# Optimization experiments

Measured on AMD Instinct MI355X. Metric: run time of the kernel, lower is better.

## Reference

```python
import jax, jax.numpy as jnp
import numpy as np

B, S, D = 2, 2048, 2048
H, HD = 16, 128
P = 2048  # past (cached) kv length


def setup_inputs() -> dict:
    key = jax.random.key(0)
    ks = jax.random.split(key, 12)
    sw = 1.0 / np.sqrt(D)
    inp = {
        "x": jax.random.normal(ks[0], (B, S, D), jnp.float32),
        "past_k": jax.random.normal(ks[1], (B, H, P, HD), jnp.float32),
        "past_v": jax.random.normal(ks[2], (B, H, P, HD), jnp.float32),
        "Wq": jax.random.normal(ks[3], (D, D), jnp.float32) * sw,
        "bq": jax.random.normal(ks[4], (D,), jnp.float32) * 0.01,
        "Wk": jax.random.normal(ks[5], (D, D), jnp.float32) * sw,
        "bk": jax.random.normal(ks[6], (D,), jnp.float32) * 0.01,
        "Wv": jax.random.normal(ks[7], (D, D), jnp.float32) * sw,
        "bv": jax.random.normal(ks[8], (D,), jnp.float32) * 0.01,
        "Wo": jax.random.normal(ks[9], (D, D), jnp.float32) * sw,
        "bo": jax.random.normal(ks[10], (D,), jnp.float32) * 0.01,
    }
    return inp


def _heads(t):
    # [B, S, D] -> [B, H, S, HD]
    return t.reshape(B, -1, H, HD).transpose(0, 2, 1, 3)


def reference(x, past_k, past_v, Wq, bq, Wk, bk, Wv, bv, Wo, bo):
    # QKV projections (separate weights, _qkv_same_embed_dim=False path)
    q = _heads(x @ Wq.T + bq)          # [B,H,S,HD]
    k_new = _heads(x @ Wk.T + bk)      # [B,H,S,HD]
    v_new = _heads(x @ Wv.T + bv)

    # KV cache append
    k_cached = jnp.concatenate([past_k, k_new], axis=2)  # [B,H,P+S,HD]
    v_cached = jnp.concatenate([past_v, v_new], axis=2)
    cached_len = P + S

    # Manual attention path (query_seq_len != cached_seq_len)
    scale = 1.0 / np.sqrt(HD)
    scores = jnp.einsum('bhqd,bhkd->bhqk', q, k_cached) * scale  # [B,H,S,P+S]
    q_pos = jnp.arange(cached_len - S, cached_len)[:, None]
    k_pos = jnp.arange(cached_len)[None, :]
    mask = q_pos >= k_pos  # offset causal mask [S, P+S]
    scores = jnp.where(mask, scores, -jnp.inf)
    attn = jax.nn.softmax(scores, axis=-1)
    out = jnp.einsum('bhqk,bhkd->bhqd', attn, v_cached)  # [B,H,S,HD]

    out = out.transpose(0, 2, 1, 3).reshape(B, S, D)
    return out @ Wo.T + bo
```

## Files before the change

kernel.cpp:

```cpp
#include <hip/hip_runtime.h>

typedef unsigned short u16;
typedef __attribute__((ext_vector_type(4))) float f32x4;
typedef __attribute__((ext_vector_type(16))) float f32x16;
typedef __attribute__((ext_vector_type(8))) short s16x8;
typedef __attribute__((ext_vector_type(2))) unsigned int u32x2v;

#define CEXP 0.12751742929f

static __device__ __forceinline__ u16 f2bf(float x) {
  unsigned u = __float_as_uint(x);
  u = u + 0x7fffu + ((u >> 16) & 1u);
  return (u16)(u >> 16);
}
static __device__ __forceinline__ unsigned cvtpk(float a, float b) {
  unsigned r;
  asm("v_cvt_pk_bf16_f32 %0, %1, %2" : "=v"(r) : "v"(a), "v"(b));
  return r;
}
static __device__ __forceinline__ u32x2v pswap(unsigned a, unsigned b) {
  return __builtin_amdgcn_permlane32_swap(a, b, false, false);
}
static __device__ __forceinline__ f32x4 fzero() { f32x4 z; z[0]=0.f; z[1]=0.f; z[2]=0.f; z[3]=0.f; return z; }
static __device__ __forceinline__ f32x4 mfma16(s16x8 a, s16x8 b, f32x4 c) {
  return __builtin_amdgcn_mfma_f32_16x16x32_bf16(a, b, c, 0, 0, 0);
}
static __device__ __forceinline__ f32x16 mfma32(s16x8 a, s16x8 b, f32x16 c) {
  return __builtin_amdgcn_mfma_f32_32x32x16_bf16(a, b, c, 0, 0, 0);
}
static __device__ __forceinline__ void gld16(const void* g, void* l) {
  __builtin_amdgcn_global_load_lds((const __attribute__((address_space(1))) void*)g,
                                   (__attribute__((address_space(3))) void*)l, 16, 0, 0);
}

__global__ void cvt_all(const float* __restrict__ x, const float* __restrict__ wq,
                        const float* __restrict__ wk, const float* __restrict__ wv,
                        const float* __restrict__ wo, const float* __restrict__ pk,
                        u16* __restrict__ xb, u16* __restrict__ wqb, u16* __restrict__ wkb,
                        u16* __restrict__ wvb, u16* __restrict__ wob, u16* __restrict__ kc) {
  int stride = gridDim.x * blockDim.x;
  for (int i4 = blockIdx.x * blockDim.x + threadIdx.x; i4 < 8388608; i4 += stride) {
    const float* s; u16* d; int i; size_t di;
    if (i4 < 2097152)      { i = i4 * 4;             s = x;  d = xb;  di = i; }
    else if (i4 < 3145728) { i = (i4 - 2097152) * 4; s = wq; d = wqb; di = i; }
    else if (i4 < 4194304) { i = (i4 - 3145728) * 4; s = wk; d = wkb; di = i; }
    else if (i4 < 5242880) { i = (i4 - 4194304) * 4; s = wv; d = wvb; di = i; }
    else if (i4 < 6291456) { i = (i4 - 5242880) * 4; s = wo; d = wob; di = i; }
    else { i = (i4 - 6291456) * 4; s = pk; d = kc; di = (size_t)i + ((size_t)(i >> 18) << 18); }
    float4 v = *reinterpret_cast<const float4*>(s + i);
    ushort4 o;
    o.x = f2bf(v.x); o.y = f2bf(v.y); o.z = f2bf(v.z); o.w = f2bf(v.w);
    *reinterpret_cast<ushort4*>(d + di) = o;
  }
}

__global__ void transpose_past_v(const float* __restrict__ src, u16* __restrict__ dst) {
  __shared__ u16 tile[64 * 138];
  int bh = blockIdx.y, pt = blockIdx.x;
  const float* s = src + ((size_t)bh * 2048 + (size_t)pt * 64) * 128;
  int t = threadIdx.x;
#pragma unroll
  for (int it = 0; it < 8; ++it) {
    int idx = it * 1024 + t * 4;
    int row = idx >> 7, col = idx & 127;
    float4 v = *reinterpret_cast<const float4*>(s + idx);
    u16* d = &tile[row * 138 + col];
    d[0] = f2bf(v.x); d[1] = f2bf(v.y); d[2] = f2bf(v.z); d[3] = f2bf(v.w);
  }
  __syncthreads();
  size_t dbase = (size_t)bh * 128 * 4096 + (size_t)pt * 64;
#pragma unroll
  for (int it = 0; it < 32; ++it) {
    int o = it * 256 + t;
    int dd = o >> 6, pos = o & 63;
    dst[dbase + (size_t)dd * 4096 + pos] = tile[pos * 138 + dd];
  }
}

__global__ void transpose_new_v(const u16* __restrict__ src, u16* __restrict__ dst) {
  __shared__ u16 tile[64 * 138];
  int bh = blockIdx.y, pt = blockIdx.x;
  const u16* s = src + ((size_t)bh * 2048 + (size_t)pt * 64) * 128;
  int t = threadIdx.x;
#pragma unroll
  for (int it = 0; it < 8; ++it) {
    int idx = it * 1024 + t * 4;
    int row = idx >> 7, col = idx & 127;
    ushort4 v = *reinterpret_cast<const ushort4*>(s + idx);
    u16* d = &tile[row * 138 + col];
    d[0] = v.x; d[1] = v.y; d[2] = v.z; d[3] = v.w;
  }
  __syncthreads();
  size_t dbase = (size_t)bh * 128 * 4096 + 2048 + (size_t)pt * 64;
#pragma unroll
  for (int it = 0; it < 32; ++it) {
    int o = it * 256 + t;
    int dd = o >> 6, pos = o & 63;
    dst[dbase + (size_t)dd * 4096 + pos] = tile[pos * 138 + dd];
  }
}

static __device__ __forceinline__ void gemm_core(const u16* __restrict__ A, const u16* __restrict__ Wn,
                                                 int m0, char* ldsb, f32x4 (&acc)[4][4]) {
  const int tid = threadIdx.x;
  const int w = tid >> 6, lane = tid & 63, g = lane >> 4, ln = lane & 15;
#pragma unroll
  for (int mi = 0; mi < 4; ++mi)
#pragma unroll
    for (int ni = 0; ni < 4; ++ni) acc[mi][ni] = fzero();

  auto stage = [&](int buf, int k0) {
#pragma unroll
    for (int i = 0; i < 2; ++i) {
      int c = w * 2 + i;
      int p = c * 1024 + lane * 16;
      int row = p >> 6;
      int colb = (p & 63) ^ ((row & 3) << 4);
      const u16* sa = A + (size_t)(m0 + row) * 2048 + k0 + (colb >> 1);
      const u16* sw = Wn + (size_t)row * 2048 + k0 + (colb >> 1);
      char* da = ldsb + buf * 16384 + c * 1024;
      gld16(sa, da);
      gld16(sw, da + 8192);
    }
  };
  stage(0, 0);
  const int wr = w >> 1, wc = w & 1;
  for (int kt = 0; kt < 64; ++kt) {
    int cur = kt & 1;
    if (kt < 63) {
      stage(cur ^ 1, (kt + 1) * 32);
      asm volatile("s_waitcnt vmcnt(4)\n\ts_barrier" ::: "memory");
    } else {
      asm volatile("s_waitcnt vmcnt(0)\n\ts_barrier" ::: "memory");
    }
    const char* bp = ldsb + cur * 16384;
    s16x8 af[4], bw[4];
#pragma unroll
    for (int mi = 0; mi < 4; ++mi) {
      int row = wr * 64 + mi * 16 + ln;
      int lin = row * 64 + g * 16;
      af[mi] = *reinterpret_cast<const s16x8*>(bp + (lin ^ ((row & 3) << 4)));
    }
#pragma unroll
    for (int ni = 0; ni < 4; ++ni) {
      int row = wc * 64 + ni * 16 + ln;
      int lin = row * 64 + g * 16;
      bw[ni] = *reinterpret_cast<const s16x8*>(bp + 8192 + (lin ^ ((row & 3) << 4)));
    }
#pragma unroll
    for (int mi = 0; mi < 4; ++mi)
#pragma unroll
      for (int ni = 0; ni < 4; ++ni)
        acc[mi][ni] = mfma16(af[mi], bw[ni], acc[mi][ni]);
    asm volatile("s_waitcnt lgkmcnt(0)\n\ts_barrier" ::: "memory");
  }
}

__global__ __launch_bounds__(256, 3) void qkv_gemm(const u16* __restrict__ xb,
    const u16* __restrict__ wq, const u16* __restrict__ wk, const u16* __restrict__ wv,
    const float* __restrict__ bq, const float* __restrict__ bk, const float* __restrict__ bv,
    u16* __restrict__ outq, u16* __restrict__ kc, u16* __restrict__ outv) {
  __shared__ char ldsb[32768];
  int m0 = blockIdx.x * 128;
  int ny = blockIdx.y;
  int wsel = ny >> 4, n0 = (ny & 15) * 128;
  const u16* W; const float* bias; u16* dst; int lrow, off;
  if (wsel == 0)      { W = wq; bias = bq; dst = outq; lrow = 2048; off = 0; }
  else if (wsel == 1) { W = wk; bias = bk; dst = kc;   lrow = 4096; off = 2048; }
  else                { W = wv; bias = bv; dst = outv; lrow = 2048; off = 0; }
  f32x4 acc[4][4];
  gemm_core(xb, W + (size_t)n0 * 2048, m0, ldsb, acc);
  const int tid = threadIdx.x, w = tid >> 6, lane = tid & 63, g = lane >> 4, ln = lane & 15;
  const int wr = w >> 1, wc = w & 1;
#pragma unroll
  for (int ni = 0; ni < 4; ++ni) {
    int j = n0 + wc * 64 + ni * 16 + ln;
    float bcol = bias[j];
    int h = j >> 7, hd = j & 127;
#pragma unroll
    for (int mi = 0; mi < 4; ++mi) {
#pragma unroll
      for (int r = 0; r < 4; ++r) {
        int rowg = m0 + wr * 64 + mi * 16 + g * 4 + r;
        int b = rowg >> 11, s = rowg & 2047;
        float val = acc[mi][ni][r] + bcol;
        dst[((size_t)(b * 16 + h) * lrow + off + s) * 128 + hd] = f2bf(val);
      }
    }
  }
}

__global__ __launch_bounds__(256, 3) void proj_gemm(const u16* __restrict__ ao, const u16* __restrict__ wo,
    const float* __restrict__ bo, float* __restrict__ out) {
  __shared__ char ldsb[32768];
  int m0 = blockIdx.x * 128, n0 = blockIdx.y * 128;
  f32x4 acc[4][4];
  gemm_core(ao, wo + (size_t)n0 * 2048, m0, ldsb, acc);
  const int tid = threadIdx.x, w = tid >> 6, lane = tid & 63, g = lane >> 4, ln = lane & 15;
  const int wr = w >> 1, wc = w & 1;
#pragma unroll
  for (int ni = 0; ni < 4; ++ni) {
    int j = n0 + wc * 64 + ni * 16 + ln;
    float bcol = bo[j];
#pragma unroll
    for (int mi = 0; mi < 4; ++mi) {
#pragma unroll
      for (int r = 0; r < 4; ++r) {
        int rowg = m0 + wr * 64 + mi * 16 + g * 4 + r;
        out[(size_t)rowg * 2048 + j] = acc[mi][ni][r] + bcol;
      }
    }
  }
}

__global__ __launch_bounds__(256, 2) void attn_kernel(const u16* __restrict__ Qb,
    const u16* __restrict__ Kc, const u16* __restrict__ Vt, u16* __restrict__ Ao) {
  __shared__ char lds[65536];
  const int tid = threadIdx.x, w = tid >> 6, lane = tid & 63;
  const int hi = lane >> 5, l5 = lane & 31;
  const int bh = blockIdx.x;
  const int qy = blockIdx.y;
  const int qbk = (qy & 8) ? (15 - (qy & 7)) : qy;
  const int b = bh >> 4, h = bh & 15;
  const u16* Qbh = Qb + (size_t)bh * 2048 * 128;
  const u16* Kbh = Kc + (size_t)bh * 4096 * 128;
  const u16* Vbh = Vt + (size_t)bh * 128 * 4096;

  const int qrow0 = qbk * 128 + w * 32;
  const int qp = 2048 + qrow0 + l5;
  const int qpmin = 2048 + qrow0;
  const int ntiles = (2048 + qbk * 128 + 128) >> 6;

  s16x8 qf[8];
#pragma unroll
  for (int kc = 0; kc < 8; ++kc)
    qf[kc] = *reinterpret_cast<const s16x8*>(Qbh + (size_t)(qrow0 + l5) * 128 + kc * 16 + hi * 8);

  s16x8 ones;
#pragma unroll
  for (int j = 0; j < 8; ++j) ones[j] = (short)0x3F80;

  f32x16 o[4], o_l;
#pragma unroll
  for (int dt = 0; dt < 4; ++dt)
#pragma unroll
    for (int i = 0; i < 16; ++i) o[dt][i] = 0.f;
#pragma unroll
  for (int i = 0; i < 16; ++i) o_l[i] = 0.f;
  float mrun = -3e38f;

  auto stage = [&](int buf, int kv0) {
    char* base = lds + buf * 32768;
#pragma unroll
    for (int i = 0; i < 4; ++i) {
      int cc = w * 4 + i;
      int f = 2 * cc + hi;
      int rh = f >> 4, kcf = (f >> 1) & 7, fh = f & 1;
      gld16(Kbh + (size_t)(kv0 + rh * 32 + l5) * 128 + kcf * 16 + fh * 8,
            base + cc * 1024);
      int g2 = 2 * cc + hi;
      int dt = g2 >> 3, c2 = (g2 >> 1) & 3, gh = g2 & 1;
      gld16(Vbh + (size_t)(dt * 32 + l5) * 4096 + kv0 + c2 * 16 + gh * 8,
            base + 16384 + cc * 1024);
    }
  };

  stage(0, 0);
  for (int t = 0; t < ntiles; ++t) {
    const int kv0 = t * 64;
    const int cur = t & 1;
    if (t + 1 < ntiles) {
      stage(cur ^ 1, kv0 + 64);
      asm volatile("s_waitcnt vmcnt(8)\n\ts_barrier" ::: "memory");
    } else {
      asm volatile("s_waitcnt vmcnt(0)\n\ts_barrier" ::: "memory");
    }
    const char* Kl = lds + cur * 32768;
    const char* Vl = Kl + 16384;
    if (kv0 <= qpmin + 31) {
      f32x16 s0, s1;
#pragma unroll
      for (int i = 0; i < 16; ++i) { s0[i] = 0.f; s1[i] = 0.f; }
      __builtin_amdgcn_s_setprio(1);
#pragma unroll
      for (int kc = 0; kc < 8; ++kc) {
        s16x8 a0 = *reinterpret_cast<const s16x8*>(Kl + kc * 1024 + lane * 16);
        s16x8 a1 = *reinterpret_cast<const s16x8*>(Kl + 8192 + kc * 1024 + lane * 16);
        s0 = mfma32(a0, qf[kc], s0);
        s1 = mfma32(a1, qf[kc], s1);
      }
      __builtin_amdgcn_s_setprio(0);
      if (kv0 + 63 > qpmin) {
#pragma unroll
        for (int i = 0; i < 16; ++i) {
          int r0 = (i & 3) + 8 * (i >> 2) + 4 * hi;
          if (kv0 + r0 > qp) s0[i] = -3e38f;
          if (kv0 + 32 + r0 > qp) s1[i] = -3e38f;
        }
      }
      float pm = fmaxf(s0[0], s0[1]);
#pragma unroll
      for (int i = 2; i < 16; i += 2) pm = fmaxf(fmaxf(pm, s0[i]), s0[i + 1]);
#pragma unroll
      for (int i = 0; i < 16; i += 2) pm = fmaxf(fmaxf(pm, s1[i]), s1[i + 1]);
      {
        u32x2v rr = pswap(__float_as_uint(pm), __float_as_uint(pm));
        pm = fmaxf(pm, __uint_as_float(hi ? rr[0] : rr[1]));
      }
      float mnew = (pm > mrun + 8.f) ? pm : mrun;
      float fsc = exp2f((mrun - mnew) * CEXP);
      mrun = mnew;
#pragma unroll
      for (int i = 0; i < 16; ++i) s0[i] = exp2f((s0[i] - mnew) * CEXP);
#pragma unroll
      for (int i = 0; i < 16; ++i) s1[i] = exp2f((s1[i] - mnew) * CEXP);
      if (!__all(fsc == 1.f)) {
#pragma unroll
        for (int dt = 0; dt < 4; ++dt)
#pragma unroll
          for (int i = 0; i < 16; ++i) o[dt][i] *= fsc;
        o_l[0] *= fsc;
      }
      s16x8 pb[4];
#pragma unroll
      for (int c2 = 0; c2 < 4; ++c2) {
        const f32x16& sv = (c2 & 2) ? s1 : s0;
        const int b0 = (c2 & 1) * 8;
        unsigned x0 = cvtpk(sv[b0 + 0], sv[b0 + 1]);
        unsigned x1 = cvtpk(sv[b0 + 2], sv[b0 + 3]);
        unsigned y0 = cvtpk(sv[b0 + 4], sv[b0 + 5]);
        unsigned y1 = cvtpk(sv[b0 + 6], sv[b0 + 7]);
        u32x2v q0 = pswap(x0, y0);
        u32x2v q1 = pswap(x1, y1);
        union { unsigned u[4]; s16x8 v; } pu;
        pu.u[0] = q0[0]; pu.u[1] = q1[0]; pu.u[2] = q0[1]; pu.u[3] = q1[1];
        pb[c2] = pu.v;
      }
      __builtin_amdgcn_s_setprio(1);
#pragma unroll
      for (int dt = 0; dt < 4; ++dt) {
#pragma unroll
        for (int c2 = 0; c2 < 4; ++c2) {
          s16x8 va = *reinterpret_cast<const s16x8*>(Vl + dt * 4096 + c2 * 1024 + lane * 16);
          o[dt] = mfma32(va, pb[c2], o[dt]);
        }
      }
#pragma unroll
      for (int c2 = 0; c2 < 4; ++c2) o_l = mfma32(ones, pb[c2], o_l);
      __builtin_amdgcn_s_setprio(0);
    }
    asm volatile("s_waitcnt lgkmcnt(0)\n\ts_barrier" ::: "memory");
  }

  float li = 1.f / o_l[0];
#pragma unroll
  for (int dt = 0; dt < 4; ++dt)
#pragma unroll
    for (int i = 0; i < 16; ++i) o[dt][i] *= li;
  const int qb = w * 32 + l5;
#pragma unroll
  for (int dt = 0; dt < 4; ++dt) {
#pragma unroll
    for (int rg = 0; rg < 4; ++rg) {
      int d0 = dt * 32 + rg * 8 + hi * 4;
      unsigned w0 = cvtpk(o[dt][rg * 4 + 0], o[dt][rg * 4 + 1]);
      unsigned w1 = cvtpk(o[dt][rg * 4 + 2], o[dt][rg * 4 + 3]);
      int lin = qb * 256 + d0 * 2;
      int phys = lin ^ ((qb & 7) << 4);
      *reinterpret_cast<uint2*>(lds + phys) = make_uint2(w0, w1);
    }
  }
  __syncthreads();
  const int qr = tid >> 4, c16 = tid & 15;
#pragma unroll
  for (int it = 0; it < 8; ++it) {
    int q = qr + it * 16;
    int phys = (q * 256 + c16 * 16) ^ ((q & 7) << 4);
    s16x8 v = *reinterpret_cast<const s16x8*>(lds + phys);
    *reinterpret_cast<s16x8*>(Ao + ((size_t)(b * 2048 + qbk * 128 + q)) * 2048 + h * 128 + c16 * 8) = v;
  }
}

extern "C" void kernel_launch(void* const* d_in, const int* in_sizes, int n_in,
                              void* d_out, int out_size, void* d_ws, size_t ws_size,
                              hipStream_t stream) {
  const float* x      = (const float*)d_in[0];
  const float* past_k = (const float*)d_in[1];
  const float* past_v = (const float*)d_in[2];
  const float* Wq = (const float*)d_in[3];
  const float* bq = (const float*)d_in[4];
  const float* Wk = (const float*)d_in[5];
  const float* bk = (const float*)d_in[6];
  const float* Wv = (const float*)d_in[7];
  const float* bv = (const float*)d_in[8];
  const float* Wo = (const float*)d_in[9];
  const float* bo = (const float*)d_in[10];
  float* out = (float*)d_out;

  char* ws = (char*)d_ws;
  u16* xb   = (u16*)(ws);
  u16* wqb  = (u16*)(ws + 16777216);
  u16* wkb  = (u16*)(ws + 25165824);
  u16* wvb  = (u16*)(ws + 33554432);
  u16* wob  = (u16*)(ws + 41943040);
  u16* kc   = (u16*)(ws + 50331648);
  u16* qbuf = (u16*)(ws + 83886080);
  u16* vn   = (u16*)(ws + 100663296);
  u16* vt   = (u16*)(ws + 117440512);
  u16* ao   = xb;

  cvt_all<<<2048, 256, 0, stream>>>(x, Wq, Wk, Wv, Wo, past_k, xb, wqb, wkb, wvb, wob, kc);
  transpose_past_v<<<dim3(32, 32), 256, 0, stream>>>(past_v, vt);
  qkv_gemm<<<dim3(32, 48), 256, 0, stream>>>(xb, wqb, wkb, wvb, bq, bk, bv, qbuf, kc, vn);
  transpose_new_v<<<dim3(32, 32), 256, 0, stream>>>(vn, vt);
  attn_kernel<<<dim3(32, 16), 256, 0, stream>>>(qbuf, kc, vt, ao);
  proj_gemm<<<dim3(32, 16), 256, 0, stream>>>(ao, wob, bo, out);
}
```

Baseline: 376.9 us.

## Pre-swizzle V into MFMA fragment order and load it directly into registers

The V transpose kernels now write V in a per-tile, per-lane fragment layout that matches the MFMA operand order. The attention kernel then loads V straight from global memory into registers each tile instead of staging it through LDS, which halves its LDS footprint to only K buffers. The aim is to cut LDS traffic and shared memory use, possibly allowing more occupancy. The cost is 16 extra vector registers of V per tile, and the V loads are issued in the same iteration they are used, so their latency is less well hidden.

```diff
diff --git a/kernel.cpp b/kernel.cpp
--- a/kernel.cpp
+++ b/kernel.cpp
@@ -55,7 +55,7 @@
 }
 
 __global__ void transpose_past_v(const float* __restrict__ src, u16* __restrict__ dst) {
-  __shared__ u16 tile[64 * 138];
+  __shared__ u16 tl[64 * 138];
   int bh = blockIdx.y, pt = blockIdx.x;
   const float* s = src + ((size_t)bh * 2048 + (size_t)pt * 64) * 128;
   int t = threadIdx.x;
@@ -64,21 +64,28 @@
     int idx = it * 1024 + t * 4;
     int row = idx >> 7, col = idx & 127;
     float4 v = *reinterpret_cast<const float4*>(s + idx);
-    u16* d = &tile[row * 138 + col];
+    u16* d = &tl[row * 138 + col];
     d[0] = f2bf(v.x); d[1] = f2bf(v.y); d[2] = f2bf(v.z); d[3] = f2bf(v.w);
   }
   __syncthreads();
-  size_t dbase = (size_t)bh * 128 * 4096 + (size_t)pt * 64;
-#pragma unroll
-  for (int it = 0; it < 32; ++it) {
-    int o = it * 256 + t;
-    int dd = o >> 6, pos = o & 63;
-    dst[dbase + (size_t)dd * 4096 + pos] = tile[pos * 138 + dd];
+  size_t obase = ((size_t)bh * 64 + pt) * 8192;
+#pragma unroll
+  for (int it = 0; it < 4; ++it) {
+    int flat = it * 2048 + t * 8;
+    int c = flat >> 9, rem = flat & 511;
+    int lam = rem >> 3;
+    int hi2 = lam >> 5, l52 = lam & 31;
+    int dt = c >> 2, c2 = c & 3;
+    union { u16 v[8]; s16x8 x; } u;
+#pragma unroll
+    for (int j = 0; j < 8; ++j)
+      u.v[j] = tl[(c2 * 16 + hi2 * 8 + j) * 138 + dt * 32 + l52];
+    *reinterpret_cast<s16x8*>(dst + obase + flat) = u.x;
   }
 }
 
 __global__ void transpose_new_v(const u16* __restrict__ src, u16* __restrict__ dst) {
-  __shared__ u16 tile[64 * 138];
+  __shared__ u16 tl[64 * 138];
   int bh = blockIdx.y, pt = blockIdx.x;
   const u16* s = src + ((size_t)bh * 2048 + (size_t)pt * 64) * 128;
   int t = threadIdx.x;
@@ -87,16 +94,23 @@
     int idx = it * 1024 + t * 4;
     int row = idx >> 7, col = idx & 127;
     ushort4 v = *reinterpret_cast<const ushort4*>(s + idx);
-    u16* d = &tile[row * 138 + col];
+    u16* d = &tl[row * 138 + col];
     d[0] = v.x; d[1] = v.y; d[2] = v.z; d[3] = v.w;
   }
   __syncthreads();
-  size_t dbase = (size_t)bh * 128 * 4096 + 2048 + (size_t)pt * 64;
-#pragma unroll
-  for (int it = 0; it < 32; ++it) {
-    int o = it * 256 + t;
-    int dd = o >> 6, pos = o & 63;
-    dst[dbase + (size_t)dd * 4096 + pos] = tile[pos * 138 + dd];
+  size_t obase = ((size_t)bh * 64 + 32 + pt) * 8192;
+#pragma unroll
+  for (int it = 0; it < 4; ++it) {
+    int flat = it * 2048 + t * 8;
+    int c = flat >> 9, rem = flat & 511;
+    int lam = rem >> 3;
+    int hi2 = lam >> 5, l52 = lam & 31;
+    int dt = c >> 2, c2 = c & 3;
+    union { u16 v[8]; s16x8 x; } u;
+#pragma unroll
+    for (int j = 0; j < 8; ++j)
+      u.v[j] = tl[(c2 * 16 + hi2 * 8 + j) * 138 + dt * 32 + l52];
+    *reinterpret_cast<s16x8*>(dst + obase + flat) = u.x;
   }
 }
 
@@ -214,8 +228,8 @@
 }
 
 __global__ __launch_bounds__(256, 2) void attn_kernel(const u16* __restrict__ Qb,
-    const u16* __restrict__ Kc, const u16* __restrict__ Vt, u16* __restrict__ Ao) {
-  __shared__ char lds[65536];
+    const u16* __restrict__ Kc, const u16* __restrict__ Vtf, u16* __restrict__ Ao) {
+  __shared__ char lds[32768];
   const int tid = threadIdx.x, w = tid >> 6, lane = tid & 63;
   const int hi = lane >> 5, l5 = lane & 31;
   const int bh = blockIdx.x;
@@ -224,7 +238,6 @@
   const int b = bh >> 4, h = bh & 15;
   const u16* Qbh = Qb + (size_t)bh * 2048 * 128;
   const u16* Kbh = Kc + (size_t)bh * 4096 * 128;
-  const u16* Vbh = Vt + (size_t)bh * 128 * 4096;
 
   const int qrow0 = qbk * 128 + w * 32;
   const int qp = 2048 + qrow0 + l5;
@@ -249,8 +262,8 @@
   for (int i = 0; i < 16; ++i) o_l[i] = 0.f;
   float mrun = -3e38f;
 
-  auto stage = [&](int buf, int kv0) {
-    char* base = lds + buf * 32768;
+  auto stageK = [&](int buf, int kv0) {
+    char* base = lds + buf * 16384;
 #pragma unroll
     for (int i = 0; i < 4; ++i) {
       int cc = w * 4 + i;
@@ -258,25 +271,25 @@
       int rh = f >> 4, kcf = (f >> 1) & 7, fh = f & 1;
       gld16(Kbh + (size_t)(kv0 + rh * 32 + l5) * 128 + kcf * 16 + fh * 8,
             base + cc * 1024);
-      int g2 = 2 * cc + hi;
-      int dt = g2 >> 3, c2 = (g2 >> 1) & 3, gh = g2 & 1;
-      gld16(Vbh + (size_t)(dt * 32 + l5) * 4096 + kv0 + c2 * 16 + gh * 8,
-            base + 16384 + cc * 1024);
     }
   };
 
-  stage(0, 0);
+  stageK(0, 0);
   for (int t = 0; t < ntiles; ++t) {
     const int kv0 = t * 64;
     const int cur = t & 1;
+    s16x8 vf[16];
+    const u16* vtb = Vtf + ((size_t)(bh * 64 + t) * 16) * 512;
+#pragma unroll
+    for (int c = 0; c < 16; ++c)
+      vf[c] = *reinterpret_cast<const s16x8*>(vtb + c * 512 + lane * 8);
     if (t + 1 < ntiles) {
-      stage(cur ^ 1, kv0 + 64);
-      asm volatile("s_waitcnt vmcnt(8)\n\ts_barrier" ::: "memory");
+      stageK(cur ^ 1, kv0 + 64);
+      asm volatile("s_waitcnt vmcnt(20)\n\ts_barrier" ::: "memory");
     } else {
-      asm volatile("s_waitcnt vmcnt(0)\n\ts_barrier" ::: "memory");
-    }
-    const char* Kl = lds + cur * 32768;
-    const char* Vl = Kl + 16384;
+      asm volatile("s_waitcnt vmcnt(16)\n\ts_barrier" ::: "memory");
+    }
+    const char* Kl = lds + cur * 16384;
     if (kv0 <= qpmin + 31) {
       f32x16 s0, s1;
 #pragma unroll
@@ -340,10 +353,8 @@
 #pragma unroll
       for (int dt = 0; dt < 4; ++dt) {
 #pragma unroll
-        for (int c2 = 0; c2 < 4; ++c2) {
-          s16x8 va = *reinterpret_cast<const s16x8*>(Vl + dt * 4096 + c2 * 1024 + lane * 16);
-          o[dt] = mfma32(va, pb[c2], o[dt]);
-        }
+        for (int c2 = 0; c2 < 4; ++c2)
+          o[dt] = mfma32(vf[dt * 4 + c2], pb[c2], o[dt]);
       }
 #pragma unroll
       for (int c2 = 0; c2 < 4; ++c2) o_l = mfma32(ones, pb[c2], o_l);
@@ -406,13 +417,13 @@
   u16* kc   = (u16*)(ws + 50331648);
   u16* qbuf = (u16*)(ws + 83886080);
   u16* vn   = (u16*)(ws + 100663296);
-  u16* vt   = (u16*)(ws + 117440512);
+  u16* vtf  = (u16*)(ws + 117440512);
   u16* ao   = xb;
 
   cvt_all<<<2048, 256, 0, stream>>>(x, Wq, Wk, Wv, Wo, past_k, xb, wqb, wkb, wvb, wob, kc);
-  transpose_past_v<<<dim3(32, 32), 256, 0, stream>>>(past_v, vt);
+  transpose_past_v<<<dim3(32, 32), 256, 0, stream>>>(past_v, vtf);
   qkv_gemm<<<dim3(32, 48), 256, 0, stream>>>(xb, wqb, wkb, wvb, bq, bk, bv, qbuf, kc, vn);
-  transpose_new_v<<<dim3(32, 32), 256, 0, stream>>>(vn, vt);
-  attn_kernel<<<dim3(32, 16), 256, 0, stream>>>(qbuf, kc, vt, ao);
+  transpose_new_v<<<dim3(32, 32), 256, 0, stream>>>(vn, vtf);
+  attn_kernel<<<dim3(32, 16), 256, 0, stream>>>(qbuf, kc, vtf, ao);
   proj_gemm<<<dim3(32, 16), 256, 0, stream>>>(ao, wob, bo, out);
 }
```

Measured after the change: 397.7 us. +5.5%, slower.
